# Performance work log

Measured on AMD Instinct MI355X. Metric: run time of the kernel, lower is better.

Reference implementation:

```python
import jax, jax.numpy as jnp
import numpy as np

N_NODES = 100000
N_EDGES = 3200000


def _gat_conv(x, src, dst, ea, Wx, We, a_src, a_dst, a_edge, b, n):
    # PyG GATConv, heads=1, edge_dim set: h = x@Wx^T, he = ea@We^T
    h = x @ Wx.T                      # [N,16]
    he = ea @ We.T                    # [E,16]
    alpha = h[src] @ a_src + h[dst] @ a_dst + he @ a_edge  # [E]
    alpha = jnp.where(alpha > 0, alpha, 0.2 * alpha)       # leaky_relu(0.2)
    m = jax.ops.segment_max(alpha, dst, num_segments=n)
    m = jnp.where(jnp.isfinite(m), m, 0.0)
    ex = jnp.exp(alpha - m[dst])
    s = jax.ops.segment_sum(ex, dst, num_segments=n)
    a = ex / (s[dst] + 1e-16)
    out = jax.ops.segment_sum(a[:, None] * h[src], dst, num_segments=n)
    return out + b


def setup_inputs() -> dict:
    key = jax.random.key(0)
    ks = iter(jax.random.split(key, 40))
    rn = lambda shape, s=0.1: jax.random.normal(next(ks), shape, dtype=jnp.float32) * s
    inp = {}
    inp['x'] = jax.random.normal(next(ks), (N_NODES, 4), dtype=jnp.float32)
    inp['edge_index'] = jax.random.randint(next(ks), (2, N_EDGES), 0, N_NODES, dtype=jnp.int64)
    inp['edge_attr'] = jax.random.normal(next(ks), (N_EDGES, 6), dtype=jnp.float32)
    # conv1: GATConv(4->16, edge_dim=6)
    inp['c1_Wx'] = rn((16, 4)); inp['c1_We'] = rn((16, 6))
    inp['c1_asrc'] = rn((16,)); inp['c1_adst'] = rn((16,)); inp['c1_aedge'] = rn((16,))
    inp['c1_b'] = rn((16,))
    # edge1 MLP: 38->32->64->32->16
    inp['e1_w1'] = rn((32, 38)); inp['e1_b1'] = rn((32,))
    inp['e1_w2'] = rn((64, 32)); inp['e1_b2'] = rn((64,))
    inp['e1_w3'] = rn((32, 64)); inp['e1_b3'] = rn((32,))
    inp['e1_w4'] = rn((16, 32)); inp['e1_b4'] = rn((16,))
    # conv2: GATConv(16->16, edge_dim=16)
    inp['c2_Wx'] = rn((16, 16)); inp['c2_We'] = rn((16, 16))
    inp['c2_asrc'] = rn((16,)); inp['c2_adst'] = rn((16,)); inp['c2_aedge'] = rn((16,))
    inp['c2_b'] = rn((16,))
    # node head 16->16->2, edge head 16->16->4
    inp['nl_w1'] = rn((16, 16)); inp['nl_b1'] = rn((16,))
    inp['nl_w2'] = rn((2, 16)); inp['nl_b2'] = rn((2,))
    inp['el_w1'] = rn((16, 16)); inp['el_b1'] = rn((16,))
    inp['el_w2'] = rn((4, 16)); inp['el_b2'] = rn((4,))
    return inp


def reference(x, edge_index, edge_attr,
              c1_Wx, c1_We, c1_asrc, c1_adst, c1_aedge, c1_b,
              e1_w1, e1_b1, e1_w2, e1_b2, e1_w3, e1_b3, e1_w4, e1_b4,
              c2_Wx, c2_We, c2_asrc, c2_adst, c2_aedge, c2_b,
              nl_w1, nl_b1, nl_w2, nl_b2,
              el_w1, el_b1, el_w2, el_b2):
    n = x.shape[0]
    src, dst = edge_index[0], edge_index[1]
    x1 = _gat_conv(x, src, dst, edge_attr, c1_Wx, c1_We, c1_asrc, c1_adst, c1_aedge, c1_b, n)
    # edge MLP on [x_src | edge_attr | x_dst] (dropout = identity in eval)
    e = jnp.concatenate([x1[src], edge_attr, x1[dst]], axis=1)  # [E,38]
    e = jax.nn.relu(e @ e1_w1.T + e1_b1)
    e = jax.nn.relu(e @ e1_w2.T + e1_b2)
    e = jax.nn.relu(e @ e1_w3.T + e1_b3)
    e = e @ e1_w4.T + e1_b4                                     # [E,16]
    x2 = _gat_conv(x1, src, dst, e, c2_Wx, c2_We, c2_asrc, c2_adst, c2_aedge, c2_b, n)
    node = jax.nn.relu(jax.nn.relu(x2 @ nl_w1.T + nl_b1) @ nl_w2.T + nl_b2)
    edge = jax.nn.relu(jax.nn.relu(e @ el_w1.T + el_b1) @ el_w2.T + el_b2)
    return (jax.nn.log_softmax(node, axis=1), jax.nn.log_softmax(edge, axis=1))
```

## Files before the change

kernel.cpp:

```cpp
#include <hip/hip_runtime.h>

#define NN 100000
#define NE 3200000
#define NB 98

typedef unsigned int u32;
typedef unsigned short u16;
typedef _Float16 f16x2 __attribute__((ext_vector_type(2)));
typedef __fp16 fp16v2 __attribute__((ext_vector_type(2)));

__device__ __forceinline__ int clampi(int s){
  s = s < 0 ? 0 : s;
  return s >= NN ? NN-1 : s;
}

__device__ __forceinline__ f16x2 pk2(float x, float y){
  fp16v2 r = __builtin_amdgcn_cvt_pkrtz(x, y);
  return __builtin_bit_cast(f16x2, r);
}
__device__ __forceinline__ float dot2(f16x2 a, f16x2 b, float c){
  return __builtin_amdgcn_fdot2(a, b, c, false);
}
__device__ __forceinline__ float f16lo(u32 w){
  __fp16 h = __builtin_bit_cast(__fp16, (u16)(w & 0xffffu));
  return (float)h;
}
__device__ __forceinline__ float f16hi(u32 w){
  __fp16 h = __builtin_bit_cast(__fp16, (u16)(w >> 16));
  return (float)h;
}
__device__ __forceinline__ float f16u(u16 w){
  __fp16 h = __builtin_bit_cast(__fp16, w);
  return (float)h;
}

template<int N4>
__device__ __forceinline__ float dotl(const float* __restrict__ a, const float* w){
  float acc0 = 0.f, acc1 = 0.f;
  #pragma unroll
  for (int k = 0; k < N4; k += 2){
    float4 q0 = ((const float4*)w)[k];
    acc0 += a[4*k]*q0.x + a[4*k+1]*q0.y + a[4*k+2]*q0.z + a[4*k+3]*q0.w;
    float4 q1 = ((const float4*)w)[k+1];
    acc1 += a[4*k+4]*q1.x + a[4*k+5]*q1.y + a[4*k+6]*q1.z + a[4*k+7]*q1.w;
  }
  return acc0 + acc1;
}

__global__ __launch_bounds__(256,8) void khist(const int* __restrict__ ei, int* __restrict__ cnt){
  int i = blockIdx.x*256 + threadIdx.x;
  if (i >= NE) return;
  atomicAdd(&cnt[clampi(ei[NE+i])], 1);
}

__global__ __launch_bounds__(1024) void kscanA(const int* __restrict__ cnt, int* __restrict__ bsum){
  __shared__ int wsum[16];
  int tid = threadIdx.x;
  int i = blockIdx.x*1024 + tid;
  int x = (i < NN) ? cnt[i] : 0;
  #pragma unroll
  for (int ofs = 1; ofs < 64; ofs <<= 1) x += __shfl_xor(x, ofs, 64);
  if ((tid & 63) == 0) wsum[tid >> 6] = x;
  __syncthreads();
  if (tid == 0){
    int t = 0;
    #pragma unroll
    for (int k = 0; k < 16; k++) t += wsum[k];
    bsum[blockIdx.x] = t;
  }
}

__global__ void kscanB(const int* __restrict__ bsum, int* __restrict__ boff, int* __restrict__ offN){
  if (threadIdx.x == 0){
    int c = 0;
    for (int b = 0; b < NB; b++){ boff[b] = c; c += bsum[b]; }
    offN[0] = c;
  }
}

__global__ __launch_bounds__(1024) void kscanC(int* __restrict__ cnt, const int* __restrict__ boff,
                                               int* __restrict__ off){
  __shared__ int wsum[16];
  int tid = threadIdx.x;
  int i = blockIdx.x*1024 + tid;
  int v = (i < NN) ? cnt[i] : 0;
  int x = v;
  #pragma unroll
  for (int ofs = 1; ofs < 64; ofs <<= 1){
    int t = __shfl_up(x, ofs, 64);
    if ((tid & 63) >= ofs) x += t;
  }
  if ((tid & 63) == 63) wsum[tid >> 6] = x;
  __syncthreads();
  if (tid < 16){
    int y = wsum[tid];
    #pragma unroll
    for (int ofs = 1; ofs < 16; ofs <<= 1){
      int t = __shfl_up(y, ofs, 64);
      if (tid >= ofs) y += t;
    }
    wsum[tid] = y;
  }
  __syncthreads();
  int wb = (tid >= 64) ? wsum[(tid >> 6) - 1] : 0;
  if (i < NN){ off[i] = boff[blockIdx.x] + wb + x - v; cnt[i] = 0; }
}

__global__ __launch_bounds__(256,4) void k1(const float* __restrict__ x,
    const float* __restrict__ Wx, const float* __restrict__ asrc, const float* __restrict__ adst,
    float* __restrict__ hs1, float* __restrict__ hd1)
{
  __shared__ float wL[64], aS[16], aD[16];
  int tid = threadIdx.x;
  if (tid < 64) wL[tid] = Wx[tid];
  if (tid < 16){ aS[tid] = asrc[tid]; aD[tid] = adst[tid]; }
  __syncthreads();
  int n = blockIdx.x*256 + tid;
  if (n >= NN) return;
  float4 xr = ((const float4*)x)[n];
  float hs=0.f, hd=0.f;
  #pragma unroll
  for (int j=0;j<16;j++){
    float h = xr.x*wL[j*4+0] + xr.y*wL[j*4+1] + xr.z*wL[j*4+2] + xr.w*wL[j*4+3];
    hs += h*aS[j]; hd += h*aD[j];
  }
  hs1[n]=hs; hd1[n]=hd;
}

__global__ __launch_bounds__(256,8) void k2a(const int* __restrict__ ei,
    const float* __restrict__ ea, const float* __restrict__ We, const float* __restrict__ aedge,
    const float* __restrict__ hs1, const float* __restrict__ hd1,
    const int* __restrict__ off, int* __restrict__ cnt, float2* __restrict__ edata)
{
  __shared__ float w6[6];
  int tid = threadIdx.x;
  if (tid < 6){
    float acc = 0.f;
    for (int j=0;j<16;j++) acc += aedge[j] * We[j*6+tid];
    w6[tid] = acc;
  }
  __syncthreads();
  int i = blockIdx.x*256 + tid;
  if (i >= NE) return;
  int s = clampi(ei[i]);
  int d = clampi(ei[NE + i]);
  const float2* eap = (const float2*)ea + (size_t)i*3;
  float2 u0 = eap[0], u1 = eap[1], u2 = eap[2];
  float al = hs1[s] + hd1[d]
    + u0.x*w6[0] + u0.y*w6[1] + u1.x*w6[2]
    + u1.y*w6[3] + u2.x*w6[4] + u2.y*w6[5];
  al = al > 0.f ? al : 0.2f*al;
  float ex = __expf(al);
  int pos = off[d] + atomicAdd(&cnt[d], 1);
  edata[pos] = make_float2(ex, __int_as_float(s));
}

__global__ __launch_bounds__(256,8) void kaggx(const float2* __restrict__ edata,
    const int* __restrict__ off, const float* __restrict__ x,
    float* __restrict__ acc4, float* __restrict__ s, int* __restrict__ cnt)
{
  int t = blockIdx.x*256 + threadIdx.x;
  int n = t >> 4;
  int j = t & 15;
  if (n >= NN) return;
  int f = j & 3, ks = j >> 2;
  int beg = off[n], end = off[n+1];
  float aj = 0.f, sl = 0.f;
  for (int k = beg + ks; k < end; k += 4){
    float2 p = edata[k];
    int src = __float_as_int(p.y);
    aj += p.x * x[(size_t)src*4 + f];
    sl += p.x;
  }
  aj += __shfl_xor(aj, 4, 64); aj += __shfl_xor(aj, 8, 64);
  sl += __shfl_xor(sl, 4, 64); sl += __shfl_xor(sl, 8, 64);
  if (ks == 0) acc4[(size_t)n*4 + f] = aj;
  if (j == 0){ s[n] = sl; cnt[n] = 0; }
}

__global__ __launch_bounds__(256,8) void kagg2(const float2* __restrict__ edata,
    const int* __restrict__ off, const u16* __restrict__ hpk,
    float* __restrict__ acc, float* __restrict__ s, int* __restrict__ cnt)
{
  int t = blockIdx.x*256 + threadIdx.x;
  int n = t >> 6;
  int l = t & 63;
  if (n >= NN) return;
  int j = l & 15, ks = l >> 4;
  int beg = off[n], end = off[n+1];
  float aj = 0.f, sl = 0.f;
  for (int k = beg + ks; k < end; k += 4){
    float2 p = edata[k];
    int src = __float_as_int(p.y);
    aj += p.x * f16u(hpk[(size_t)src*16 + j]);
    sl += p.x;
  }
  aj += __shfl_xor(aj, 16, 64); aj += __shfl_xor(aj, 32, 64);
  sl += __shfl_xor(sl, 16, 64); sl += __shfl_xor(sl, 32, 64);
  if (ks == 0) acc[(size_t)n*16 + j] = aj;
  if (l == 0){ s[n] = sl; cnt[n] = 0; }
}

__global__ __launch_bounds__(256,2) void k4(const float* __restrict__ acc4,
    const float* __restrict__ sb, const float* __restrict__ c1b,
    const float* __restrict__ Wx1, const float* __restrict__ Wx2,
    const float* __restrict__ a2s, const float* __restrict__ a2d,
    const float* __restrict__ w1p,
    u32* __restrict__ hpk,
    float* __restrict__ hs2, float* __restrict__ hd2,
    u32* __restrict__ uh, u32* __restrict__ vh)
{
  __shared__ float wL[256], bL[16], aS[16], aD[16], w0L[64];
  __shared__ float w1sL[32*16], w1dL[32*16];
  int tid = threadIdx.x;
  wL[tid] = Wx2[tid];
  if (tid < 64) w0L[tid] = Wx1[tid];
  if (tid < 16){ bL[tid]=c1b[tid]; aS[tid]=a2s[tid]; aD[tid]=a2d[tid]; }
  for (int idx=tid; idx<512; idx+=256){
    int j=idx>>4, k=idx&15;
    w1sL[idx] = w1p[j*38+k];
    w1dL[idx] = w1p[j*38+22+k];
  }
  __syncthreads();
  int n = blockIdx.x*256 + tid;
  if (n >= NN) return;
  float inv = 1.f/(sb[n] + 1e-16f);
  float4 a4 = ((const float4*)acc4)[n];
  float m0 = a4.x*inv, m1 = a4.y*inv, m2 = a4.z*inv, m3 = a4.w*inv;
  float xv[16];
  #pragma unroll
  for (int j=0;j<16;j++)
    xv[j] = m0*w0L[j*4+0] + m1*w0L[j*4+1] + m2*w0L[j*4+2] + m3*w0L[j*4+3] + bL[j];
  float hs=0.f, hd=0.f;
  float hv[16];
  #pragma unroll
  for (int j=0;j<16;j++){
    float acc = 0.f;
    #pragma unroll
    for (int k=0;k<16;k++) acc += xv[k]*wL[j*16+k];
    hv[j] = acc; hs += acc*aS[j]; hd += acc*aD[j];
  }
  u32* hr = hpk + (size_t)n*8;
  #pragma unroll
  for (int j=0;j<8;j++) hr[j] = __builtin_bit_cast(u32, pk2(hv[2*j], hv[2*j+1]));
  hs2[n]=hs; hd2[n]=hd;
  u32* ur = uh + (size_t)n*16;
  u32* vr = vh + (size_t)n*16;
  #pragma unroll
  for (int j=0;j<16;j++){
    float u0 = dotl<4>(xv, &w1sL[(2*j)*16]);
    float u1 = dotl<4>(xv, &w1sL[(2*j+1)*16]);
    ur[j] = __builtin_bit_cast(u32, pk2(u0, u1));
    float v0 = dotl<4>(xv, &w1dL[(2*j)*16]);
    float v1 = dotl<4>(xv, &w1dL[(2*j+1)*16]);
    vr[j] = __builtin_bit_cast(u32, pk2(v0, v1));
  }
}

__global__ __launch_bounds__(256,5) void k5(
    const int* __restrict__ ei, const float* __restrict__ ea,
    const u32* __restrict__ uh, const u32* __restrict__ vh,
    const float* __restrict__ hs2, const float* __restrict__ hd2,
    const float* w1p, const float* b1p, const float* w2p, const float* b2p,
    const float* w3p, const float* b3p, const float* w4p, const float* b4p,
    const float* We2, const float* a2e,
    const float* ew1p, const float* eb1p, const float* ew2p, const float* eb2p,
    const int* __restrict__ off, int* __restrict__ cnt, float2* __restrict__ edata,
    float* __restrict__ eout)
{
  __shared__ __align__(16) f16x2 w1eh[32*4];  __shared__ float b1L[32];
  __shared__ __align__(16) f16x2 w2h[64*16];  __shared__ float b2L[64];
  __shared__ __align__(16) f16x2 w3h[32*32];  __shared__ float b3L[32];
  __shared__ __align__(16) f16x2 w4h[16*16];  __shared__ float b4L[16];
  __shared__ __align__(16) f16x2 ew1h[16*8];  __shared__ float eb1L[16];
  __shared__ __align__(16) f16x2 ew2h[4*8];   __shared__ float eb2L[4];
  __shared__ __align__(16) f16x2 w16h[8];
  int tid = threadIdx.x;
  if (tid < 128){
    int j=tid>>2, kk=tid&3;
    int k0=2*kk, k1=2*kk+1;
    float v0 = (k0<6) ? w1p[j*38+16+k0] : 0.f;
    float v1 = (k1<6) ? w1p[j*38+16+k1] : 0.f;
    w1eh[tid] = pk2(v0, v1);
  }
  for (int idx=tid; idx<1024; idx+=256){
    int j=idx>>4, kk=idx&15;
    w2h[idx] = pk2(w2p[j*32+2*kk], w2p[j*32+2*kk+1]);
  }
  for (int idx=tid; idx<1024; idx+=256){
    int j=idx>>5, kk=idx&31;
    w3h[idx] = pk2(w3p[j*64+2*kk], w3p[j*64+2*kk+1]);
  }
  if (tid < 256){
    int j=tid>>4, kk=tid&15;
    w4h[tid] = pk2(w4p[j*32+2*kk], w4p[j*32+2*kk+1]);
  }
  if (tid < 128){
    int j=tid>>3, kk=tid&7;
    ew1h[tid] = pk2(ew1p[j*16+2*kk], ew1p[j*16+2*kk+1]);
  }
  if (tid < 32){
    int j=tid>>3, kk=tid&7;
    ew2h[tid] = pk2(ew2p[j*16+2*kk], ew2p[j*16+2*kk+1]);
  }
  if (tid < 8){
    float s0=0.f, s1=0.f;
    for (int j=0;j<16;j++){
      s0 += a2e[j] * We2[j*16 + 2*tid];
      s1 += a2e[j] * We2[j*16 + 2*tid + 1];
    }
    w16h[tid] = pk2(s0, s1);
  }
  if (tid < 64) b2L[tid] = b2p[tid];
  if (tid < 32){ b1L[tid] = b1p[tid]; b3L[tid] = b3p[tid]; }
  if (tid < 16){ b4L[tid] = b4p[tid]; eb1L[tid] = eb1p[tid]; }
  if (tid < 4)  eb2L[tid] = eb2p[tid];
  __syncthreads();

  int i = blockIdx.x*256 + tid;
  if (i >= NE) return;
  int s = clampi(ei[i]);
  int d = clampi(ei[NE + i]);

  f16x2 a1h[16];
  {
    const float2* eap = (const float2*)ea + (size_t)i*3;
    float2 e0=eap[0], e1=eap[1], e2=eap[2];
    f16x2 eh[4];
    eh[0]=pk2(e0.x,e0.y); eh[1]=pk2(e1.x,e1.y); eh[2]=pk2(e2.x,e2.y); eh[3]=pk2(0.f,0.f);
    const uint4* up = (const uint4*)(uh + (size_t)s*16);
    const uint4* vp = (const uint4*)(vh + (size_t)d*16);
    uint4 U[4], V[4];
    #pragma unroll
    for (int q=0;q<4;q++){ U[q]=up[q]; V[q]=vp[q]; }
    u32 uw[16], vw[16];
    #pragma unroll
    for (int q=0;q<4;q++){
      uw[4*q]=U[q].x; uw[4*q+1]=U[q].y; uw[4*q+2]=U[q].z; uw[4*q+3]=U[q].w;
      vw[4*q]=V[q].x; vw[4*q+1]=V[q].y; vw[4*q+2]=V[q].z; vw[4*q+3]=V[q].w;
    }
    #pragma unroll
    for (int j=0;j<16;j++){
      float t0 = b1L[2*j]   + f16lo(uw[j]) + f16lo(vw[j]);
      float t1 = b1L[2*j+1] + f16hi(uw[j]) + f16hi(vw[j]);
      #pragma unroll
      for (int kk=0;kk<4;kk++){
        t0 = dot2(eh[kk], w1eh[(2*j)*4+kk],   t0);
        t1 = dot2(eh[kk], w1eh[(2*j+1)*4+kk], t1);
      }
      a1h[j] = pk2(fmaxf(t0,0.f), fmaxf(t1,0.f));
    }
  }
  f16x2 a2h[32];
  #pragma unroll
  for (int j=0;j<32;j++){
    float acc0 = b2L[2*j], acc1 = b2L[2*j+1];
    #pragma unroll
    for (int kk=0;kk<16;kk++){
      acc0 = dot2(a1h[kk], w2h[(2*j)*16+kk],   acc0);
      acc1 = dot2(a1h[kk], w2h[(2*j+1)*16+kk], acc1);
    }
    a2h[j] = pk2(fmaxf(acc0,0.f), fmaxf(acc1,0.f));
  }
  f16x2 a3h[16];
  #pragma unroll
  for (int j=0;j<16;j++){
    float acc0 = b3L[2*j], acc1 = b3L[2*j+1];
    #pragma unroll
    for (int kk=0;kk<32;kk++){
      acc0 = dot2(a2h[kk], w3h[(2*j)*32+kk],   acc0);
      acc1 = dot2(a2h[kk], w3h[(2*j+1)*32+kk], acc1);
    }
    a3h[j] = pk2(fmaxf(acc0,0.f), fmaxf(acc1,0.f));
  }
  f16x2 eh4[8];
  #pragma unroll
  for (int j=0;j<8;j++){
    float acc0 = b4L[2*j], acc1 = b4L[2*j+1];
    #pragma unroll
    for (int kk=0;kk<16;kk++){
      acc0 = dot2(a3h[kk], w4h[(2*j)*16+kk],   acc0);
      acc1 = dot2(a3h[kk], w4h[(2*j+1)*16+kk], acc1);
    }
    eh4[j] = pk2(acc0, acc1);
  }
  f16x2 th[8];
  #pragma unroll
  for (int j=0;j<8;j++){
    float acc0 = eb1L[2*j], acc1 = eb1L[2*j+1];
    #pragma unroll
    for (int kk=0;kk<8;kk++){
      acc0 = dot2(eh4[kk], ew1h[(2*j)*8+kk],   acc0);
      acc1 = dot2(eh4[kk], ew1h[(2*j+1)*8+kk], acc1);
    }
    th[j] = pk2(fmaxf(acc0,0.f), fmaxf(acc1,0.f));
  }
  float y0 = eb2L[0], y1 = eb2L[1], y2 = eb2L[2], y3 = eb2L[3];
  #pragma unroll
  for (int kk=0;kk<8;kk++){
    y0 = dot2(th[kk], ew2h[0*8+kk], y0);
    y1 = dot2(th[kk], ew2h[1*8+kk], y1);
    y2 = dot2(th[kk], ew2h[2*8+kk], y2);
    y3 = dot2(th[kk], ew2h[3*8+kk], y3);
  }
  y0 = fmaxf(y0,0.f); y1 = fmaxf(y1,0.f); y2 = fmaxf(y2,0.f); y3 = fmaxf(y3,0.f);
  float m = fmaxf(fmaxf(y0,y1), fmaxf(y2,y3));
  float l = m + __logf(__expf(y0-m)+__expf(y1-m)+__expf(y2-m)+__expf(y3-m));
  float4 eo; eo.x = y0-l; eo.y = y1-l; eo.z = y2-l; eo.w = y3-l;
  ((float4*)eout)[i] = eo;

  float al = hs2[s] + hd2[d];
  #pragma unroll
  for (int kk=0;kk<8;kk++) al = dot2(eh4[kk], w16h[kk], al);
  al = al > 0.f ? al : 0.2f*al;
  float ex = __expf(al);
  int pos = off[d] + atomicAdd(&cnt[d], 1);
  edata[pos] = make_float2(ex, __int_as_float(s));
}

__global__ __launch_bounds__(256,4) void k7(const float* __restrict__ accb,
    const float* __restrict__ sb, const float* __restrict__ c2b,
    const float* __restrict__ w1p, const float* __restrict__ b1p,
    const float* __restrict__ w2p, const float* __restrict__ b2p,
    float* __restrict__ nout)
{
  __shared__ float wL[256], bL[16], w2L[32], b2L[2], cb[16];
  int tid = threadIdx.x;
  wL[tid] = w1p[tid];
  if (tid < 16){ bL[tid]=b1p[tid]; cb[tid]=c2b[tid]; }
  if (tid < 32) w2L[tid] = w2p[tid];
  if (tid < 2)  b2L[tid] = b2p[tid];
  __syncthreads();
  int n = blockIdx.x*256 + tid;
  if (n >= NN) return;
  float inv = 1.f/(sb[n] + 1e-16f);
  const float* xp = accb + (size_t)n*16;
  float v[16];
  #pragma unroll
  for (int j=0;j<16;j++) v[j] = xp[j]*inv + cb[j];
  float t[16];
  #pragma unroll
  for (int j=0;j<16;j++){
    float acc = bL[j];
    #pragma unroll
    for (int k=0;k<16;k++) acc += v[k]*wL[j*16+k];
    t[j] = fmaxf(acc, 0.f);
  }
  float y0 = b2L[0], y1 = b2L[1];
  #pragma unroll
  for (int k=0;k<16;k++){ y0 += t[k]*w2L[k]; y1 += t[k]*w2L[16+k]; }
  y0 = fmaxf(y0, 0.f); y1 = fmaxf(y1, 0.f);
  float m = fmaxf(y0, y1);
  float l = m + __logf(__expf(y0-m) + __expf(y1-m));
  float2 no; no.x = y0-l; no.y = y1-l;
  ((float2*)nout)[n] = no;
}

extern "C" void kernel_launch(void* const* d_in, const int* in_sizes, int n_in,
                              void* d_out, int out_size, void* d_ws, size_t ws_size,
                              hipStream_t stream)
{
  const float* x  = (const float*)d_in[0];
  const int* ei   = (const int*)d_in[1];
  const float* ea = (const float*)d_in[2];
  const float* c1Wx = (const float*)d_in[3];
  const float* c1We = (const float*)d_in[4];
  const float* c1as = (const float*)d_in[5];
  const float* c1ad = (const float*)d_in[6];
  const float* c1ae = (const float*)d_in[7];
  const float* c1b  = (const float*)d_in[8];
  const float* e1w1 = (const float*)d_in[9];
  const float* e1b1 = (const float*)d_in[10];
  const float* e1w2 = (const float*)d_in[11];
  const float* e1b2 = (const float*)d_in[12];
  const float* e1w3 = (const float*)d_in[13];
  const float* e1b3 = (const float*)d_in[14];
  const float* e1w4 = (const float*)d_in[15];
  const float* e1b4 = (const float*)d_in[16];
  const float* c2Wx = (const float*)d_in[17];
  const float* c2We = (const float*)d_in[18];
  const float* c2as = (const float*)d_in[19];
  const float* c2ad = (const float*)d_in[20];
  const float* c2ae = (const float*)d_in[21];
  const float* c2b  = (const float*)d_in[22];
  const float* nlw1 = (const float*)d_in[23];
  const float* nlb1 = (const float*)d_in[24];
  const float* nlw2 = (const float*)d_in[25];
  const float* nlb2 = (const float*)d_in[26];
  const float* elw1 = (const float*)d_in[27];
  const float* elb1 = (const float*)d_in[28];
  const float* elw2 = (const float*)d_in[29];
  const float* elb2 = (const float*)d_in[30];

  float* ws = (float*)d_ws;
  const size_t N = NN;
  int* off   = (int*)ws;
  int* cnt   = (int*)ws + (N + 8);
  int* bsum  = (int*)ws + (2*N + 8);
  int* boff  = (int*)ws + (2*N + 136);
  u32* hpk   = (u32*)(ws + 2*N + 264);
  float* hs  = ws + 10*N + 264;
  float* hd  = hs + N;
  float* acc = hd + N;
  float* acc4= acc + 16*N;
  float* s   = acc4 + 4*N;
  u32* uh    = (u32*)(s + N);
  u32* vh    = uh + 16*N;
  float2* edata = (float2*)(vh + 16*N);

  float* nout = (float*)d_out;
  float* eout = (float*)d_out + 200000;

  const int GE = (NE + 255)/256;
  const int GN = (NN + 255)/256;

  (void)hipMemsetAsync(cnt, 0, N*sizeof(int), stream);
  khist<<<GE, 256, 0, stream>>>(ei, cnt);
  kscanA<<<NB, 1024, 0, stream>>>(cnt, bsum);
  kscanB<<<1, 64, 0, stream>>>(bsum, boff, off + NN);
  kscanC<<<NB, 1024, 0, stream>>>(cnt, boff, off);
  k1<<<GN, 256, 0, stream>>>(x, c1Wx, c1as, c1ad, hs, hd);
  k2a<<<GE, 256, 0, stream>>>(ei, ea, c1We, c1ae, hs, hd, off, cnt, edata);
  kaggx<<<(NN*16 + 255)/256, 256, 0, stream>>>(edata, off, x, acc4, s, cnt);
  k4<<<GN, 256, 0, stream>>>(acc4, s, c1b, c1Wx, c2Wx, c2as, c2ad, e1w1, hpk, hs, hd, uh, vh);
  k5<<<GE, 256, 0, stream>>>(ei, ea, uh, vh, hs, hd,
      e1w1, e1b1, e1w2, e1b2, e1w3, e1b3, e1w4, e1b4,
      c2We, c2ae, elw1, elb1, elw2, elb2,
      off, cnt, edata, eout);
  kagg2<<<(NN*64 + 255)/256, 256, 0, stream>>>(edata, off, (const u16*)hpk, acc, s, cnt);
  k7<<<GN, 256, 0, stream>>>(acc, s, c2b, nlw1, nlb1, nlw2, nlb2, nout);
}
```

Baseline: 745.2 us.

## Replace layer-1 CSR aggregation with float atomics and fuse node head into kagg2

The first GAT layer no longer scatters edges into the CSR buffer followed by a separate gather kernel. k2a now atomically adds ex and ex*x[src] straight into per-node sum and acc4 buffers, which kscanC zeroes. The second aggregation kernel kagg2 also computes the node MLP and log-softmax with wave shuffles, which removes k7 and the 16-wide acc buffer round trip. The cost is 5 float atomics per edge with contention on dst nodes and a nondeterministic summation order.

```diff
diff --git a/kernel.cpp b/kernel.cpp
--- a/kernel.cpp
+++ b/kernel.cpp
@@ -79,7 +79,8 @@
 }
 
 __global__ __launch_bounds__(1024) void kscanC(int* __restrict__ cnt, const int* __restrict__ boff,
-                                               int* __restrict__ off){
+                                               int* __restrict__ off,
+                                               float* __restrict__ acc4, float* __restrict__ s){
   __shared__ int wsum[16];
   int tid = threadIdx.x;
   int i = blockIdx.x*1024 + tid;
@@ -103,7 +104,13 @@
   }
   __syncthreads();
   int wb = (tid >= 64) ? wsum[(tid >> 6) - 1] : 0;
-  if (i < NN){ off[i] = boff[blockIdx.x] + wb + x - v; cnt[i] = 0; }
+  if (i < NN){
+    off[i] = boff[blockIdx.x] + wb + x - v;
+    cnt[i] = 0;
+    s[i] = 0.f;
+    float4 z; z.x=z.y=z.z=z.w=0.f;
+    ((float4*)acc4)[i] = z;
+  }
 }
 
 __global__ __launch_bounds__(256,4) void k1(const float* __restrict__ x,
@@ -130,7 +137,8 @@
 __global__ __launch_bounds__(256,8) void k2a(const int* __restrict__ ei,
     const float* __restrict__ ea, const float* __restrict__ We, const float* __restrict__ aedge,
     const float* __restrict__ hs1, const float* __restrict__ hd1,
-    const int* __restrict__ off, int* __restrict__ cnt, float2* __restrict__ edata)
+    const float* __restrict__ x,
+    float* __restrict__ acc4, float* __restrict__ s1)
 {
   __shared__ float w6[6];
   int tid = threadIdx.x;
@@ -151,54 +159,13 @@
     + u1.y*w6[3] + u2.x*w6[4] + u2.y*w6[5];
   al = al > 0.f ? al : 0.2f*al;
   float ex = __expf(al);
-  int pos = off[d] + atomicAdd(&cnt[d], 1);
-  edata[pos] = make_float2(ex, __int_as_float(s));
-}
-
-__global__ __launch_bounds__(256,8) void kaggx(const float2* __restrict__ edata,
-    const int* __restrict__ off, const float* __restrict__ x,
-    float* __restrict__ acc4, float* __restrict__ s, int* __restrict__ cnt)
-{
-  int t = blockIdx.x*256 + threadIdx.x;
-  int n = t >> 4;
-  int j = t & 15;
-  if (n >= NN) return;
-  int f = j & 3, ks = j >> 2;
-  int beg = off[n], end = off[n+1];
-  float aj = 0.f, sl = 0.f;
-  for (int k = beg + ks; k < end; k += 4){
-    float2 p = edata[k];
-    int src = __float_as_int(p.y);
-    aj += p.x * x[(size_t)src*4 + f];
-    sl += p.x;
-  }
-  aj += __shfl_xor(aj, 4, 64); aj += __shfl_xor(aj, 8, 64);
-  sl += __shfl_xor(sl, 4, 64); sl += __shfl_xor(sl, 8, 64);
-  if (ks == 0) acc4[(size_t)n*4 + f] = aj;
-  if (j == 0){ s[n] = sl; cnt[n] = 0; }
-}
-
-__global__ __launch_bounds__(256,8) void kagg2(const float2* __restrict__ edata,
-    const int* __restrict__ off, const u16* __restrict__ hpk,
-    float* __restrict__ acc, float* __restrict__ s, int* __restrict__ cnt)
-{
-  int t = blockIdx.x*256 + threadIdx.x;
-  int n = t >> 6;
-  int l = t & 63;
-  if (n >= NN) return;
-  int j = l & 15, ks = l >> 4;
-  int beg = off[n], end = off[n+1];
-  float aj = 0.f, sl = 0.f;
-  for (int k = beg + ks; k < end; k += 4){
-    float2 p = edata[k];
-    int src = __float_as_int(p.y);
-    aj += p.x * f16u(hpk[(size_t)src*16 + j]);
-    sl += p.x;
-  }
-  aj += __shfl_xor(aj, 16, 64); aj += __shfl_xor(aj, 32, 64);
-  sl += __shfl_xor(sl, 16, 64); sl += __shfl_xor(sl, 32, 64);
-  if (ks == 0) acc[(size_t)n*16 + j] = aj;
-  if (l == 0){ s[n] = sl; cnt[n] = 0; }
+  float4 xs = ((const float4*)x)[s];
+  unsafeAtomicAdd(&s1[d], ex);
+  float* a4 = acc4 + (size_t)d*4;
+  unsafeAtomicAdd(a4+0, ex*xs.x);
+  unsafeAtomicAdd(a4+1, ex*xs.y);
+  unsafeAtomicAdd(a4+2, ex*xs.z);
+  unsafeAtomicAdd(a4+3, ex*xs.w);
 }
 
 __global__ __launch_bounds__(256,2) void k4(const float* __restrict__ acc4,
@@ -418,42 +385,60 @@
   edata[pos] = make_float2(ex, __int_as_float(s));
 }
 
-__global__ __launch_bounds__(256,4) void k7(const float* __restrict__ accb,
-    const float* __restrict__ sb, const float* __restrict__ c2b,
+__global__ __launch_bounds__(256,8) void kagg2(const float2* __restrict__ edata,
+    const int* __restrict__ off, const u16* __restrict__ hpk,
+    const float* __restrict__ c2b,
     const float* __restrict__ w1p, const float* __restrict__ b1p,
     const float* __restrict__ w2p, const float* __restrict__ b2p,
-    float* __restrict__ nout)
+    float* __restrict__ nout, int* __restrict__ cnt)
 {
-  __shared__ float wL[256], bL[16], w2L[32], b2L[2], cb[16];
-  int tid = threadIdx.x;
-  wL[tid] = w1p[tid];
-  if (tid < 16){ bL[tid]=b1p[tid]; cb[tid]=c2b[tid]; }
+  __shared__ float w1L[256], cb[16], b1L[16], w2L[32], b2L[2];
+  int tid = threadIdx.x;
+  w1L[tid] = w1p[tid];
+  if (tid < 16){ cb[tid] = c2b[tid]; b1L[tid] = b1p[tid]; }
   if (tid < 32) w2L[tid] = w2p[tid];
   if (tid < 2)  b2L[tid] = b2p[tid];
   __syncthreads();
-  int n = blockIdx.x*256 + tid;
+  int t = blockIdx.x*256 + tid;
+  int n = t >> 6;
+  int l = t & 63;
   if (n >= NN) return;
-  float inv = 1.f/(sb[n] + 1e-16f);
-  const float* xp = accb + (size_t)n*16;
-  float v[16];
-  #pragma unroll
-  for (int j=0;j<16;j++) v[j] = xp[j]*inv + cb[j];
-  float t[16];
-  #pragma unroll
-  for (int j=0;j<16;j++){
-    float acc = bL[j];
-    #pragma unroll
-    for (int k=0;k<16;k++) acc += v[k]*wL[j*16+k];
-    t[j] = fmaxf(acc, 0.f);
-  }
-  float y0 = b2L[0], y1 = b2L[1];
-  #pragma unroll
-  for (int k=0;k<16;k++){ y0 += t[k]*w2L[k]; y1 += t[k]*w2L[16+k]; }
-  y0 = fmaxf(y0, 0.f); y1 = fmaxf(y1, 0.f);
-  float m = fmaxf(y0, y1);
-  float l = m + __logf(__expf(y0-m) + __expf(y1-m));
-  float2 no; no.x = y0-l; no.y = y1-l;
-  ((float2*)nout)[n] = no;
+  int j = l & 15, ks = l >> 4;
+  int beg = off[n], end = off[n+1];
+  float aj = 0.f, sl = 0.f;
+  for (int k = beg + ks; k < end; k += 4){
+    float2 p = edata[k];
+    int src = __float_as_int(p.y);
+    aj += p.x * f16u(hpk[(size_t)src*16 + j]);
+    sl += p.x;
+  }
+  aj += __shfl_xor(aj, 16, 64); aj += __shfl_xor(aj, 32, 64);
+  sl += __shfl_xor(sl, 16, 64); sl += __shfl_xor(sl, 32, 64);
+  float inv = 1.f/(sl + 1e-16f);
+  float vj = aj*inv + cb[j];
+  float tj = b1L[j];
+  #pragma unroll
+  for (int k=0;k<16;k++){
+    float vk = __shfl(vj, k, 16);
+    tj += vk * w1L[j*16 + k];
+  }
+  tj = fmaxf(tj, 0.f);
+  float p0 = tj * w2L[j];
+  float p1 = tj * w2L[16 + j];
+  #pragma unroll
+  for (int ofs=1; ofs<16; ofs<<=1){
+    p0 += __shfl_xor(p0, ofs, 64);
+    p1 += __shfl_xor(p1, ofs, 64);
+  }
+  if (l == 0){
+    float y0 = fmaxf(p0 + b2L[0], 0.f);
+    float y1 = fmaxf(p1 + b2L[1], 0.f);
+    float m = fmaxf(y0, y1);
+    float lg = m + __logf(__expf(y0-m) + __expf(y1-m));
+    float2 no; no.x = y0-lg; no.y = y1-lg;
+    ((float2*)nout)[n] = no;
+    cnt[n] = 0;
+  }
 }
 
 extern "C" void kernel_launch(void* const* d_in, const int* in_sizes, int n_in,
@@ -501,8 +486,7 @@
   u32* hpk   = (u32*)(ws + 2*N + 264);
   float* hs  = ws + 10*N + 264;
   float* hd  = hs + N;
-  float* acc = hd + N;
-  float* acc4= acc + 16*N;
+  float* acc4= hd + N;
   float* s   = acc4 + 4*N;
   u32* uh    = (u32*)(s + N);
   u32* vh    = uh + 16*N;
@@ -518,15 +502,14 @@
   khist<<<GE, 256, 0, stream>>>(ei, cnt);
   kscanA<<<NB, 1024, 0, stream>>>(cnt, bsum);
   kscanB<<<1, 64, 0, stream>>>(bsum, boff, off + NN);
-  kscanC<<<NB, 1024, 0, stream>>>(cnt, boff, off);
+  kscanC<<<NB, 1024, 0, stream>>>(cnt, boff, off, acc4, s);
   k1<<<GN, 256, 0, stream>>>(x, c1Wx, c1as, c1ad, hs, hd);
-  k2a<<<GE, 256, 0, stream>>>(ei, ea, c1We, c1ae, hs, hd, off, cnt, edata);
-  kaggx<<<(NN*16 + 255)/256, 256, 0, stream>>>(edata, off, x, acc4, s, cnt);
+  k2a<<<GE, 256, 0, stream>>>(ei, ea, c1We, c1ae, hs, hd, x, acc4, s);
   k4<<<GN, 256, 0, stream>>>(acc4, s, c1b, c1Wx, c2Wx, c2as, c2ad, e1w1, hpk, hs, hd, uh, vh);
   k5<<<GE, 256, 0, stream>>>(ei, ea, uh, vh, hs, hd,
       e1w1, e1b1, e1w2, e1b2, e1w3, e1b3, e1w4, e1b4,
       c2We, c2ae, elw1, elb1, elw2, elb2,
       off, cnt, edata, eout);
-  kagg2<<<(NN*64 + 255)/256, 256, 0, stream>>>(edata, off, (const u16*)hpk, acc, s, cnt);
-  k7<<<GN, 256, 0, stream>>>(acc, s, c2b, nlw1, nlb1, nlw2, nlb2, nout);
-}
+  kagg2<<<(NN*64 + 255)/256, 256, 0, stream>>>(edata, off, (const u16*)hpk,
+      c2b, nlw1, nlb1, nlw2, nlb2, nout, cnt);
+}
```

Result: slower. 1.372 ms (+84.1%).
